# Performance work log

Hardware: AMD Instinct MI355X
Metric: run time of the kernel (lower is better)

## Reference

```python
import jax, jax.numpy as jnp
import numpy as np

R = 16            # grid resolution
WIN = 8           # window size (voxels per side)
NW3 = (R // WIN) ** 3   # number of windows = 8
WS = WIN ** 3           # tokens per window = 512
N = R ** 3              # active voxels = 4096
C = 512; H = 8; DH = C // H; L = 8; LAT = 8
NG = 4; VOX = 0.015625; OUTC = 14 * NG; MLP = 4 * C


def _radical_inverse(base, i):
    f = 1.0; r = 0.0
    while i > 0:
        f /= base; r += f * (i % base); i //= base
    return r


def _offset_perturbation():
    # hammersley_sequence(3, i, NG) = [i/NG, phi_2(i), phi_3(i)]
    p = np.array([[i / NG, _radical_inverse(2, i), _radical_inverse(3, i)] for i in range(NG)], np.float32)
    p = p * 2.0 - 1.0
    p = np.clip(p / VOX, -0.99, 0.99)
    return jnp.asarray(np.arctanh(p).astype(np.float32))  # [NG, 3]


def setup_inputs() -> dict:
    key = jax.random.key(0)
    ks = jax.random.split(key, 12)
    nw = R // WIN
    # window-major voxel ordering: dense 16^3 grid grouped into 8^3 windows
    win = np.stack(np.meshgrid(*[np.arange(nw)] * 3, indexing='ij'), -1).reshape(-1, 3)
    inner = np.stack(np.meshgrid(*[np.arange(WIN)] * 3, indexing='ij'), -1).reshape(-1, 3)
    xyz = (win[:, None, :] * WIN + inner[None, :, :]).reshape(-1, 3).astype(np.int32)
    coords = jnp.asarray(np.concatenate([np.zeros((N, 1), np.int32), xyz], axis=1))  # [N,4] (batch,x,y,z)
    s = 0.02
    return {
        'feats': jax.random.normal(ks[0], (N, LAT), jnp.float32),
        'coords': coords,
        'emb_x': jax.random.normal(ks[1], (1024, C // 3), jnp.float32) * s,
        'emb_y': jax.random.normal(ks[2], (1024, C // 3), jnp.float32) * s,
        'emb_z': jax.random.normal(ks[3], (1024, C - 2 * (C // 3)), jnp.float32) * s,
        'w_in': jax.random.normal(ks[4], (LAT, C), jnp.float32) * s,
        'b_in': jnp.zeros((C,), jnp.float32),
        'ln1_g': jnp.ones((L, C), jnp.float32), 'ln1_b': jnp.zeros((L, C), jnp.float32),
        'w_qkv': jax.random.normal(ks[5], (L, C, 3 * C), jnp.float32) * s,
        'b_qkv': jnp.zeros((L, 3 * C), jnp.float32),
        'w_o': jax.random.normal(ks[6], (L, C, C), jnp.float32) * s,
        'b_o': jnp.zeros((L, C), jnp.float32),
        'ln2_g': jnp.ones((L, C), jnp.float32), 'ln2_b': jnp.zeros((L, C), jnp.float32),
        'w_m1': jax.random.normal(ks[7], (L, C, MLP), jnp.float32) * s,
        'b_m1': jnp.zeros((L, MLP), jnp.float32),
        'w_m2': jax.random.normal(ks[8], (L, MLP, C), jnp.float32) * s,
        'b_m2': jnp.zeros((L, C), jnp.float32),
        'w_out': jax.random.normal(ks[9], (C, OUTC), jnp.float32) * s,
        'b_out': jnp.zeros((OUTC,), jnp.float32),
        'offset_perturb': _offset_perturbation(),
    }


def _ln(x, g, b, eps):
    m = jnp.mean(x, axis=-1, keepdims=True)
    v = jnp.var(x, axis=-1, keepdims=True)
    return (x - m) * jax.lax.rsqrt(v + eps) * g + b


def _forward(feats, coords, emb_x, emb_y, emb_z, w_in, b_in, ln1_g, ln1_b,
             w_qkv, b_qkv, w_o, b_o, ln2_g, ln2_b, w_m1, b_m1, w_m2, b_m2,
             w_out, b_out, offset_perturb):
    # input_layer + absolute position embedding (gather from 3 tables)
    h = feats @ w_in + b_in  # [N, C]
    pe = jnp.concatenate([emb_x[coords[:, 1]], emb_y[coords[:, 2]], emb_z[coords[:, 3]]], axis=-1)
    h = h + pe

    def block(h, p):
        l1g, l1b, wq, bq, wo, bo, l2g, l2b, w1, b1, w2, b2 = p
        a = _ln(h, l1g, l1b, 1e-6)
        qkv = (a @ wq + bq).reshape(NW3, WS, 3, H, DH)  # voxels are window-major
        q, k, v = qkv[:, :, 0], qkv[:, :, 1], qkv[:, :, 2]
        scores = jnp.einsum('wqhd,wkhd->whqk', q, k) / jnp.sqrt(jnp.float32(DH))
        attn = jax.nn.softmax(scores, axis=-1)
        o = jnp.einsum('whqk,wkhd->wqhd', attn, v).reshape(N, C)
        h = h + o @ wo + bo
        m = _ln(h, l2g, l2b, 1e-6)
        h = h + jax.nn.gelu(m @ w1 + b1) @ w2 + b2
        return h, None

    params = (ln1_g, ln1_b, w_qkv, b_qkv, w_o, b_o, ln2_g, ln2_b, w_m1, b_m1, w_m2, b_m2)
    h, _ = jax.lax.scan(block, h, params)

    # final non-affine layer_norm + out projection
    h = _ln(h, jnp.ones((C,), h.dtype), jnp.zeros((C,), h.dtype), 1e-5)
    out = h @ w_out + b_out  # [N, 56]

    # to_representation (single batch)
    xyz_base = (coords[:, 1:].astype(jnp.float32) + 0.5) / R  # [N, 3]
    off = out[:, 0:3 * NG].reshape(N, NG, 3) + offset_perturb
    off = jnp.tanh(off) / R * 0.5 * VOX
    _xyz = (xyz_base[:, None, :] + off).reshape(N * NG, 3)
    _fdc = out[:, 3 * NG:6 * NG].reshape(N * NG, 1, 3)
    _scal = out[:, 6 * NG:9 * NG].reshape(N * NG, 3)
    _rot = out[:, 9 * NG:13 * NG].reshape(N * NG, 4)
    _opa = out[:, 13 * NG:14 * NG].reshape(N * NG, 1)
    return _xyz, _fdc, _scal, _rot, _opa


def reference(feats, coords, emb_x, emb_y, emb_z, w_in, b_in, ln1_g, ln1_b,
              w_qkv, b_qkv, w_o, b_o, ln2_g, ln2_b, w_m1, b_m1, w_m2, b_m2,
              w_out, b_out, offset_perturb):
    return _forward(feats, coords, emb_x, emb_y, emb_z, w_in, b_in, ln1_g, ln1_b,
                    w_qkv, b_qkv, w_o, b_o, ln2_g, ln2_b, w_m1, b_m1, w_m2, b_m2,
                    w_out, b_out, offset_perturb)
```

## Files before the change

### kernel.cpp

```cpp
#include <hip/hip_runtime.h>
#include <stdint.h>

typedef unsigned short u16;
typedef short bf16x8 __attribute__((ext_vector_type(8)));
typedef float f32x4 __attribute__((ext_vector_type(4)));

#define NTOK 4096
#define CDIM 512
#define NHEAD 8
#define LAYERS 8
#define MLPD 2048
#define QKVD 1536

__device__ __forceinline__ u16 f2bf(float f){
  union { float f; unsigned u; } c; c.f = f;
  return (u16)((c.u + 0x7FFFu + ((c.u >> 16) & 1u)) >> 16);
}

__device__ __forceinline__ void llds16(const void* g, void* l){
  __builtin_amdgcn_global_load_lds((const __attribute__((address_space(1))) void*)g,
                                   (__attribute__((address_space(3))) void*)l, 16, 0, 0);
}

__global__ void kt_transpose(const float* __restrict__ W, u16* __restrict__ Wt, int K, int N){
  __shared__ float tile[32][33];
  int l = blockIdx.z;
  W  += (size_t)l * K * N;
  Wt += (size_t)l * K * N;
  int k0 = blockIdx.y * 32, n0 = blockIdx.x * 32;
  int t = threadIdx.x;
  int r = t >> 3, c4 = (t & 7) << 2;
  float4 v = *(const float4*)&W[(size_t)(k0 + r) * N + n0 + c4];
  tile[r][c4 + 0] = v.x; tile[r][c4 + 1] = v.y; tile[r][c4 + 2] = v.z; tile[r][c4 + 3] = v.w;
  __syncthreads();
  ushort4 o;
  o.x = f2bf(tile[c4 + 0][r]);
  o.y = f2bf(tile[c4 + 1][r]);
  o.z = f2bf(tile[c4 + 2][r]);
  o.w = f2bf(tile[c4 + 3][r]);
  *(ushort4*)&Wt[(size_t)(n0 + r) * K + k0 + c4] = o;
}

__global__ void kt_embed(const float* __restrict__ feats, const int* __restrict__ coords,
                         const float* __restrict__ ex, const float* __restrict__ ey,
                         const float* __restrict__ ez, const float* __restrict__ w_in,
                         const float* __restrict__ b_in, float* __restrict__ h){
  __shared__ float fs[8];
  __shared__ int cc[3];
  int n = blockIdx.x, t = threadIdx.x;
  if (t < 8) fs[t] = feats[n * 8 + t];
  if (t == 8) { cc[0] = coords[n*4+1]; cc[1] = coords[n*4+2]; cc[2] = coords[n*4+3]; }
  __syncthreads();
  for (int c = t; c < CDIM; c += 256){
    float acc = b_in[c];
    #pragma unroll
    for (int i = 0; i < 8; i++) acc += fs[i] * w_in[i * CDIM + c];
    float pe;
    if (c < 170)      pe = ex[cc[0] * 170 + c];
    else if (c < 340) pe = ey[cc[1] * 170 + (c - 170)];
    else              pe = ez[cc[2] * 172 + (c - 340)];
    h[(size_t)n * CDIM + c] = acc + pe;
  }
}

__global__ void kt_ln(const float* __restrict__ h, const float* __restrict__ g,
                      const float* __restrict__ b, u16* __restrict__ out, float eps){
  int wave = threadIdx.x >> 6, lane = threadIdx.x & 63;
  int row = blockIdx.x * 4 + wave;
  const float* hr = h + (size_t)row * CDIM + lane * 8;
  float4 v0 = *(const float4*)hr, v1 = *(const float4*)(hr + 4);
  float x[8] = {v0.x, v0.y, v0.z, v0.w, v1.x, v1.y, v1.z, v1.w};
  float s = 0.f, q = 0.f;
  #pragma unroll
  for (int i = 0; i < 8; i++){ s += x[i]; q += x[i] * x[i]; }
  #pragma unroll
  for (int off = 32; off; off >>= 1){ s += __shfl_xor(s, off); q += __shfl_xor(q, off); }
  float mean = s * (1.0f / CDIM);
  float var  = q * (1.0f / CDIM) - mean * mean;
  float rr = rsqrtf(var + eps);
  int cb = lane * 8;
  u16 u[8];
  #pragma unroll
  for (int i = 0; i < 8; i++)
    u[i] = f2bf((x[i] - mean) * rr * g[cb + i] + b[cb + i]);
  uint4 pk;
  pk.x = (unsigned)u[0] | ((unsigned)u[1] << 16);
  pk.y = (unsigned)u[2] | ((unsigned)u[3] << 16);
  pk.z = (unsigned)u[4] | ((unsigned)u[5] << 16);
  pk.w = (unsigned)u[6] | ((unsigned)u[7] << 16);
  *(uint4*)&out[(size_t)row * CDIM + cb] = pk;
}

template<int BM, int BN, int MODE>
__global__ __launch_bounds__(256) void kt_gemm(
    const u16* __restrict__ A, const u16* __restrict__ Wt, const float* __restrict__ bias,
    u16* __restrict__ outb, float* __restrict__ hres, u16* __restrict__ vT, int N, int K)
{
  constexpr int MF = BM / 32;
  constexpr int NF = BN / 32;
  __shared__ __align__(16) u16 As[2][BM * 64];
  __shared__ __align__(16) u16 Bs[2][BN * 64];
  int tid = threadIdx.x, wave = tid >> 6, lane = tid & 63;
  int m0 = blockIdx.y * BM, n0 = blockIdx.x * BN;
  int wm = wave >> 1, wn = wave & 1;
  f32x4 acc[MF][NF];
  const f32x4 fzero = {0.f, 0.f, 0.f, 0.f};
  #pragma unroll
  for (int m = 0; m < MF; m++)
    #pragma unroll
    for (int n = 0; n < NF; n++) acc[m][n] = fzero;

  int srow = lane >> 3;
  int sblk = (lane & 7) ^ srow;
  const u16* gA = A  + (size_t)(m0 + wave * 8 + srow) * K + sblk * 8;
  const u16* gB = Wt + (size_t)(n0 + wave * 8 + srow) * K + sblk * 8;

  auto stage = [&](int buf, int kt){
    #pragma unroll
    for (int j = 0; j < BM / 32; j++)
      llds16(gA + (size_t)(j * 32) * K + kt, &As[buf][(j * 32 + wave * 8) * 64]);
    #pragma unroll
    for (int j = 0; j < BN / 32; j++)
      llds16(gB + (size_t)(j * 32) * K + kt, &Bs[buf][(j * 32 + wave * 8) * 64]);
  };

  int nk = K >> 6;
  stage(0, 0);
  __syncthreads();
  int rl = lane & 15, hg = lane >> 4;
  for (int t = 0; t < nk; ++t){
    int cur = t & 1;
    if (t + 1 < nk) stage(cur ^ 1, (t + 1) << 6);
    #pragma unroll
    for (int kk = 0; kk < 2; kk++){
      bf16x8 af[MF], bfr[NF];
      int bl = (kk << 2) + hg;
      #pragma unroll
      for (int m = 0; m < MF; m++){
        int row = wm * (BM / 2) + m * 16 + rl;
        af[m] = *(const bf16x8*)&As[cur][row * 64 + ((bl ^ (row & 7)) << 3)];
      }
      #pragma unroll
      for (int n = 0; n < NF; n++){
        int row = wn * (BN / 2) + n * 16 + rl;
        bfr[n] = *(const bf16x8*)&Bs[cur][row * 64 + ((bl ^ (row & 7)) << 3)];
      }
      #pragma unroll
      for (int m = 0; m < MF; m++)
        #pragma unroll
        for (int n = 0; n < NF; n++)
          acc[m][n] = __builtin_amdgcn_mfma_f32_16x16x32_bf16(af[m], bfr[n], acc[m][n], 0, 0, 0);
    }
    __syncthreads();
  }

  int cl = lane & 15, rg = lane >> 4;
  #pragma unroll
  for (int m = 0; m < MF; m++){
    int row0 = m0 + wm * (BM / 2) + m * 16 + rg * 4;
    #pragma unroll
    for (int n = 0; n < NF; n++){
      int col = n0 + wn * (BN / 2) + n * 16 + cl;
      float bb = bias[col];
      if (MODE == 1){
        #pragma unroll
        for (int r = 0; r < 4; r++){
          size_t idx = (size_t)(row0 + r) * N + col;
          hres[idx] += acc[m][n][r] + bb;
        }
      } else if (MODE == 2){
        #pragma unroll
        for (int r = 0; r < 4; r++){
          float x = acc[m][n][r] + bb;
          float t = 0.7978845608028654f * (x + 0.044715f * x * x * x);
          outb[(size_t)(row0 + r) * N + col] = f2bf(0.5f * x * (1.0f + tanhf(t)));
        }
      } else {
        if (col < 1024){
          #pragma unroll
          for (int r = 0; r < 4; r++)
            outb[(size_t)(row0 + r) * N + col] = f2bf(acc[m][n][r] + bb);
        } else {
          int dh = col - 1024;
          int win = row0 >> 9, tin = row0 & 511;
          ushort4 p;
          p.x = f2bf(acc[m][n][0] + bb);
          p.y = f2bf(acc[m][n][1] + bb);
          p.z = f2bf(acc[m][n][2] + bb);
          p.w = f2bf(acc[m][n][3] + bb);
          *(ushort4*)&vT[(size_t)(win * 512 + dh) * 512 + tin] = p;
        }
      }
    }
  }
}

__global__ __launch_bounds__(256) void kt_attn(const u16* __restrict__ qkv,
                                               const u16* __restrict__ vT,
                                               u16* __restrict__ o){
  __shared__ __align__(16) u16 P[4][32 * 32];
  int tid = threadIdx.x, wave = tid >> 6, lane = tid & 63;
  int qc = blockIdx.x, head = blockIdx.y, win = blockIdx.z;
  int rl = lane & 15, hg = lane >> 4;
  int qbase = win * 512 + qc * 128 + wave * 32;
  const u16* qptr = qkv + (size_t)qbase * QKVD + head * 64;
  const u16* kptr = qkv + (size_t)(win * 512) * QKVD + 512 + head * 64;
  const u16* vptr = vT + (size_t)(win * 512 + head * 64) * 512;
  u16* Pl = &P[wave][0];

  bf16x8 qf[2][2];
  #pragma unroll
  for (int m = 0; m < 2; m++)
    #pragma unroll
    for (int kk = 0; kk < 2; kk++)
      qf[m][kk] = *(const bf16x8*)(qptr + (size_t)(m * 16 + rl) * QKVD + kk * 32 + hg * 8);

  const f32x4 fzero = {0.f, 0.f, 0.f, 0.f};
  f32x4 Oa[2][4];
  float mrun[2][4], lrun[2][4];
  #pragma unroll
  for (int m = 0; m < 2; m++){
    #pragma unroll
    for (int d = 0; d < 4; d++) Oa[m][d] = fzero;
    #pragma unroll
    for (int r = 0; r < 4; r++){ mrun[m][r] = -1e30f; lrun[m][r] = 0.f; }
  }

  for (int kt = 0; kt < 512; kt += 32){
    f32x4 s[2][2];
    #pragma unroll
    for (int m = 0; m < 2; m++){ s[m][0] = fzero; s[m][1] = fzero; }
    #pragma unroll
    for (int c = 0; c < 2; c++){
      bf16x8 kf0 = *(const bf16x8*)(kptr + (size_t)(kt + c * 16 + rl) * QKVD + hg * 8);
      bf16x8 kf1 = *(const bf16x8*)(kptr + (size_t)(kt + c * 16 + rl) * QKVD + 32 + hg * 8);
      #pragma unroll
      for (int m = 0; m < 2; m++){
        s[m][c] = __builtin_amdgcn_mfma_f32_16x16x32_bf16(qf[m][0], kf0, s[m][c], 0, 0, 0);
        s[m][c] = __builtin_amdgcn_mfma_f32_16x16x32_bf16(qf[m][1], kf1, s[m][c], 0, 0, 0);
      }
    }
    bf16x8 vf[4];
    #pragma unroll
    for (int d = 0; d < 4; d++)
      vf[d] = *(const bf16x8*)(vptr + (size_t)(d * 16 + rl) * 512 + kt + hg * 8);

    #pragma unroll
    for (int m = 0; m < 2; m++){
      #pragma unroll
      for (int r = 0; r < 4; r++){
        float s0 = s[m][0][r] * 0.125f, s1 = s[m][1][r] * 0.125f;
        float mx = fmaxf(s0, s1);
        #pragma unroll
        for (int off = 1; off < 16; off <<= 1) mx = fmaxf(mx, __shfl_xor(mx, off));
        float mnew = fmaxf(mrun[m][r], mx);
        float corr = __expf(mrun[m][r] - mnew);
        mrun[m][r] = mnew;
        float p0 = __expf(s0 - mnew), p1 = __expf(s1 - mnew);
        float ps = p0 + p1;
        #pragma unroll
        for (int off = 1; off < 16; off <<= 1) ps += __shfl_xor(ps, off);
        lrun[m][r] = lrun[m][r] * corr + ps;
        #pragma unroll
        for (int d = 0; d < 4; d++) Oa[m][d][r] *= corr;
        s[m][0][r] = p0; s[m][1][r] = p1;
      }
    }
    #pragma unroll
    for (int m = 0; m < 2; m++)
      #pragma unroll
      for (int c = 0; c < 2; c++)
        #pragma unroll
        for (int r = 0; r < 4; r++){
          int row = m * 16 + hg * 4 + r;
          int colb = c * 2 + (rl >> 3);
          Pl[row * 32 + ((colb ^ (row & 3)) << 3) + (rl & 7)] = f2bf(s[m][c][r]);
        }
    __syncthreads();
    #pragma unroll
    for (int m = 0; m < 2; m++){
      int prow = m * 16 + rl;
      bf16x8 pf = *(const bf16x8*)&Pl[prow * 32 + ((hg ^ (prow & 3)) << 3)];
      #pragma unroll
      for (int d = 0; d < 4; d++)
        Oa[m][d] = __builtin_amdgcn_mfma_f32_16x16x32_bf16(pf, vf[d], Oa[m][d], 0, 0, 0);
    }
    __syncthreads();
  }
  #pragma unroll
  for (int m = 0; m < 2; m++)
    #pragma unroll
    for (int d = 0; d < 4; d++)
      #pragma unroll
      for (int r = 0; r < 4; r++){
        int row = qbase + m * 16 + hg * 4 + r;
        o[(size_t)row * CDIM + head * 64 + d * 16 + rl] = f2bf(Oa[m][d][r] / lrun[m][r]);
      }
}

__global__ void kt_final(const float* __restrict__ h, const float* __restrict__ w_out,
                         const float* __restrict__ b_out, const int* __restrict__ coords,
                         const float* __restrict__ offp, float* __restrict__ out){
  __shared__ float lnv[CDIM];
  __shared__ float ov[56];
  int n = blockIdx.x, lane = threadIdx.x;
  const float* hr = h + (size_t)n * CDIM + lane * 8;
  float4 v0 = *(const float4*)hr, v1 = *(const float4*)(hr + 4);
  float x[8] = {v0.x, v0.y, v0.z, v0.w, v1.x, v1.y, v1.z, v1.w};
  float s = 0.f, q = 0.f;
  #pragma unroll
  for (int i = 0; i < 8; i++){ s += x[i]; q += x[i] * x[i]; }
  #pragma unroll
  for (int off = 32; off; off >>= 1){ s += __shfl_xor(s, off); q += __shfl_xor(q, off); }
  float mean = s * (1.0f / CDIM);
  float var  = q * (1.0f / CDIM) - mean * mean;
  float rr = rsqrtf(var + 1e-5f);
  #pragma unroll
  for (int i = 0; i < 8; i++) lnv[lane * 8 + i] = (x[i] - mean) * rr;
  __syncthreads();
  if (lane < 56){
    float a = b_out[lane];
    for (int k = 0; k < CDIM; k++) a += lnv[k] * w_out[k * 56 + lane];
    ov[lane] = a;
  }
  __syncthreads();
  if (lane < 12){
    int g = lane / 3, d = lane - g * 3;
    float base = ((float)coords[n * 4 + 1 + d] + 0.5f) * (1.0f / 16.0f);
    float t = tanhf(ov[lane] + offp[lane]);
    out[(size_t)n * 12 + lane] = base + t * 4.8828125e-4f;
    out[49152  + (size_t)n * 12 + lane] = ov[12 + lane];
    out[98304  + (size_t)n * 12 + lane] = ov[24 + lane];
  }
  if (lane < 16) out[147456 + (size_t)n * 16 + lane] = ov[36 + lane];
  if (lane < 4)  out[212992 + (size_t)n * 4  + lane] = ov[52 + lane];
}

extern "C" void kernel_launch(void* const* d_in, const int* in_sizes, int n_in,
                              void* d_out, int out_size, void* d_ws, size_t ws_size,
                              hipStream_t stream) {
  const float* feats = (const float*)d_in[0];
  const int*   coords = (const int*)d_in[1];
  const float* emb_x = (const float*)d_in[2];
  const float* emb_y = (const float*)d_in[3];
  const float* emb_z = (const float*)d_in[4];
  const float* w_in  = (const float*)d_in[5];
  const float* b_in  = (const float*)d_in[6];
  const float* ln1_g = (const float*)d_in[7];
  const float* ln1_b = (const float*)d_in[8];
  const float* w_qkv = (const float*)d_in[9];
  const float* b_qkv = (const float*)d_in[10];
  const float* w_o   = (const float*)d_in[11];
  const float* b_o   = (const float*)d_in[12];
  const float* ln2_g = (const float*)d_in[13];
  const float* ln2_b = (const float*)d_in[14];
  const float* w_m1  = (const float*)d_in[15];
  const float* b_m1  = (const float*)d_in[16];
  const float* w_m2  = (const float*)d_in[17];
  const float* b_m2  = (const float*)d_in[18];
  const float* w_out = (const float*)d_in[19];
  const float* b_out = (const float*)d_in[20];
  const float* offp  = (const float*)d_in[21];

  char* ws = (char*)d_ws;
  auto carve = [&](size_t bytes){ char* p = ws; ws += (bytes + 255) & ~(size_t)255; return p; };
  float* h   = (float*)carve((size_t)NTOK * CDIM * 4);
  u16* a     = (u16*)carve((size_t)NTOK * CDIM * 2);
  u16* qkvb  = (u16*)carve((size_t)NTOK * QKVD * 2);
  u16* vT    = (u16*)carve((size_t)NTOK * CDIM * 2);
  u16* ob    = (u16*)carve((size_t)NTOK * CDIM * 2);
  u16* ub    = (u16*)carve((size_t)NTOK * MLPD * 2);
  u16* wqkvT = (u16*)carve((size_t)LAYERS * QKVD * CDIM * 2);
  u16* woT   = (u16*)carve((size_t)LAYERS * CDIM * CDIM * 2);
  u16* wm1T  = (u16*)carve((size_t)LAYERS * MLPD * CDIM * 2);
  u16* wm2T  = (u16*)carve((size_t)LAYERS * CDIM * MLPD * 2);

  kt_transpose<<<dim3(QKVD/32, CDIM/32, LAYERS), 256, 0, stream>>>(w_qkv, wqkvT, CDIM, QKVD);
  kt_transpose<<<dim3(CDIM/32, CDIM/32, LAYERS), 256, 0, stream>>>(w_o,   woT,   CDIM, CDIM);
  kt_transpose<<<dim3(MLPD/32, CDIM/32, LAYERS), 256, 0, stream>>>(w_m1,  wm1T,  CDIM, MLPD);
  kt_transpose<<<dim3(CDIM/32, MLPD/32, LAYERS), 256, 0, stream>>>(w_m2,  wm2T,  MLPD, CDIM);
  kt_embed<<<NTOK, 256, 0, stream>>>(feats, coords, emb_x, emb_y, emb_z, w_in, b_in, h);

  for (int l = 0; l < LAYERS; ++l){
    kt_ln<<<NTOK/4, 256, 0, stream>>>(h, ln1_g + l*CDIM, ln1_b + l*CDIM, a, 1e-6f);
    kt_gemm<64,128,0><<<dim3(QKVD/128, NTOK/64), 256, 0, stream>>>(
        a, wqkvT + (size_t)l*QKVD*CDIM, b_qkv + l*QKVD, qkvb, nullptr, vT, QKVD, CDIM);
    kt_attn<<<dim3(4, NHEAD, 8), 256, 0, stream>>>(qkvb, vT, ob);
    kt_gemm<64,64,1><<<dim3(CDIM/64, NTOK/64), 256, 0, stream>>>(
        ob, woT + (size_t)l*CDIM*CDIM, b_o + l*CDIM, nullptr, h, nullptr, CDIM, CDIM);
    kt_ln<<<NTOK/4, 256, 0, stream>>>(h, ln2_g + l*CDIM, ln2_b + l*CDIM, a, 1e-6f);
    kt_gemm<64,128,2><<<dim3(MLPD/128, NTOK/64), 256, 0, stream>>>(
        a, wm1T + (size_t)l*MLPD*CDIM, b_m1 + l*MLPD, ub, nullptr, nullptr, MLPD, CDIM);
    kt_gemm<64,64,1><<<dim3(CDIM/64, NTOK/64), 256, 0, stream>>>(
        ub, wm2T + (size_t)l*CDIM*MLPD, b_m2 + l*CDIM, nullptr, h, nullptr, CDIM, MLPD);
  }
  kt_final<<<NTOK, 64, 0, stream>>>(h, w_out, b_out, coords, offp, (float*)d_out);
}
```

Baseline: 1.019 ms.

## Restructure attention: 16-row waves, transposed S, register P shuffle, double-buffered K/V

The attention kernel now gives each wave a 16-query tile instead of 32, which raises the grid from 256 to 512 blocks (2048 wave tasks) for better occupancy. S is computed transposed (K as the A operand) so the per-row max and sum reductions need only two cross-lane shuffles. The P matrix is rearranged into the MFMA operand layout through register shuffles, removing the LDS staging buffer and both __syncthreads per tile. K and V fragments are double-buffered in registers to overlap global loads with compute. In exchange, each K/V fragment is reloaded by twice as many waves, and the shuffle-based layout is easy to get wrong.

```diff
diff --git a/kernel.cpp b/kernel.cpp
--- a/kernel.cpp
+++ b/kernel.cpp
@@ -15,6 +15,10 @@
 __device__ __forceinline__ u16 f2bf(float f){
   union { float f; unsigned u; } c; c.f = f;
   return (u16)((c.u + 0x7FFFu + ((c.u >> 16) & 1u)) >> 16);
+}
+
+__device__ __forceinline__ unsigned pack2(float a, float b){
+  return (unsigned)f2bf(a) | ((unsigned)f2bf(b) << 16);
 }
 
 __device__ __forceinline__ void llds16(const void* g, void* l){
@@ -198,104 +202,111 @@
 __global__ __launch_bounds__(256) void kt_attn(const u16* __restrict__ qkv,
                                                const u16* __restrict__ vT,
                                                u16* __restrict__ o){
-  __shared__ __align__(16) u16 P[4][32 * 32];
   int tid = threadIdx.x, wave = tid >> 6, lane = tid & 63;
-  int qc = blockIdx.x, head = blockIdx.y, win = blockIdx.z;
+  int task = blockIdx.x * 4 + wave;
+  int qc = task & 31, head = (task >> 5) & 7, win = task >> 8;
   int rl = lane & 15, hg = lane >> 4;
-  int qbase = win * 512 + qc * 128 + wave * 32;
-  const u16* qptr = qkv + (size_t)qbase * QKVD + head * 64;
+  int qbase = win * 512 + qc * 16;
+  const u16* qptr = qkv + (size_t)(qbase + rl) * QKVD + head * 64;
   const u16* kptr = qkv + (size_t)(win * 512) * QKVD + 512 + head * 64;
   const u16* vptr = vT + (size_t)(win * 512 + head * 64) * 512;
-  u16* Pl = &P[wave][0];
-
-  bf16x8 qf[2][2];
-  #pragma unroll
-  for (int m = 0; m < 2; m++)
-    #pragma unroll
-    for (int kk = 0; kk < 2; kk++)
-      qf[m][kk] = *(const bf16x8*)(qptr + (size_t)(m * 16 + rl) * QKVD + kk * 32 + hg * 8);
+
+  bf16x8 qf0 = *(const bf16x8*)(qptr + hg * 8);
+  bf16x8 qf1 = *(const bf16x8*)(qptr + 32 + hg * 8);
 
   const f32x4 fzero = {0.f, 0.f, 0.f, 0.f};
-  f32x4 Oa[2][4];
-  float mrun[2][4], lrun[2][4];
-  #pragma unroll
-  for (int m = 0; m < 2; m++){
-    #pragma unroll
-    for (int d = 0; d < 4; d++) Oa[m][d] = fzero;
-    #pragma unroll
-    for (int r = 0; r < 4; r++){ mrun[m][r] = -1e30f; lrun[m][r] = 0.f; }
-  }
-
-  for (int kt = 0; kt < 512; kt += 32){
-    f32x4 s[2][2];
-    #pragma unroll
-    for (int m = 0; m < 2; m++){ s[m][0] = fzero; s[m][1] = fzero; }
-    #pragma unroll
-    for (int c = 0; c < 2; c++){
-      bf16x8 kf0 = *(const bf16x8*)(kptr + (size_t)(kt + c * 16 + rl) * QKVD + hg * 8);
-      bf16x8 kf1 = *(const bf16x8*)(kptr + (size_t)(kt + c * 16 + rl) * QKVD + 32 + hg * 8);
+  f32x4 Oa[4] = {fzero, fzero, fzero, fzero};
+  float mrun = -1e30f, lrun = 0.f;
+
+  bf16x8 kA[2][2], vA[4], kB[2][2], vB[4];
+
+  auto loadK = [&](int kt, bf16x8 kf[2][2]){
+    #pragma unroll
+    for (int c = 0; c < 2; c++)
       #pragma unroll
-      for (int m = 0; m < 2; m++){
-        s[m][c] = __builtin_amdgcn_mfma_f32_16x16x32_bf16(qf[m][0], kf0, s[m][c], 0, 0, 0);
-        s[m][c] = __builtin_amdgcn_mfma_f32_16x16x32_bf16(qf[m][1], kf1, s[m][c], 0, 0, 0);
-      }
-    }
-    bf16x8 vf[4];
+      for (int dk = 0; dk < 2; dk++)
+        kf[c][dk] = *(const bf16x8*)(kptr + (size_t)(kt + c * 16 + rl) * QKVD + dk * 32 + hg * 8);
+  };
+  auto loadV = [&](int kt, bf16x8 vf[4]){
     #pragma unroll
     for (int d = 0; d < 4; d++)
       vf[d] = *(const bf16x8*)(vptr + (size_t)(d * 16 + rl) * 512 + kt + hg * 8);
-
-    #pragma unroll
-    for (int m = 0; m < 2; m++){
-      #pragma unroll
-      for (int r = 0; r < 4; r++){
-        float s0 = s[m][0][r] * 0.125f, s1 = s[m][1][r] * 0.125f;
-        float mx = fmaxf(s0, s1);
-        #pragma unroll
-        for (int off = 1; off < 16; off <<= 1) mx = fmaxf(mx, __shfl_xor(mx, off));
-        float mnew = fmaxf(mrun[m][r], mx);
-        float corr = __expf(mrun[m][r] - mnew);
-        mrun[m][r] = mnew;
-        float p0 = __expf(s0 - mnew), p1 = __expf(s1 - mnew);
-        float ps = p0 + p1;
-        #pragma unroll
-        for (int off = 1; off < 16; off <<= 1) ps += __shfl_xor(ps, off);
-        lrun[m][r] = lrun[m][r] * corr + ps;
-        #pragma unroll
-        for (int d = 0; d < 4; d++) Oa[m][d][r] *= corr;
-        s[m][0][r] = p0; s[m][1][r] = p1;
-      }
+  };
+
+  auto process = [&](bf16x8 kf[2][2], bf16x8 vf[4]){
+    f32x4 s0 = fzero, s1 = fzero;
+    s0 = __builtin_amdgcn_mfma_f32_16x16x32_bf16(kf[0][0], qf0, s0, 0, 0, 0);
+    s0 = __builtin_amdgcn_mfma_f32_16x16x32_bf16(kf[0][1], qf1, s0, 0, 0, 0);
+    s1 = __builtin_amdgcn_mfma_f32_16x16x32_bf16(kf[1][0], qf0, s1, 0, 0, 0);
+    s1 = __builtin_amdgcn_mfma_f32_16x16x32_bf16(kf[1][1], qf1, s1, 0, 0, 0);
+    float v[8];
+    #pragma unroll
+    for (int r = 0; r < 4; r++){ v[r] = s0[r] * 0.125f; v[4 + r] = s1[r] * 0.125f; }
+    float tmax = v[0];
+    #pragma unroll
+    for (int i = 1; i < 8; i++) tmax = fmaxf(tmax, v[i]);
+    tmax = fmaxf(tmax, __shfl_xor(tmax, 16));
+    tmax = fmaxf(tmax, __shfl_xor(tmax, 32));
+    float mnew = fmaxf(mrun, tmax);
+    float corr = __expf(mrun - mnew);
+    mrun = mnew;
+    float p[8], ps = 0.f;
+    #pragma unroll
+    for (int i = 0; i < 8; i++){ p[i] = __expf(v[i] - mnew); ps += p[i]; }
+    ps += __shfl_xor(ps, 16);
+    ps += __shfl_xor(ps, 32);
+    lrun = lrun * corr + ps;
+    float c0 = __shfl(corr, (hg << 2) + 0);
+    float c1 = __shfl(corr, (hg << 2) + 1);
+    float c2 = __shfl(corr, (hg << 2) + 2);
+    float c3 = __shfl(corr, (hg << 2) + 3);
+    #pragma unroll
+    for (int d = 0; d < 4; d++){
+      Oa[d][0] *= c0; Oa[d][1] *= c1; Oa[d][2] *= c2; Oa[d][3] *= c3;
     }
-    #pragma unroll
-    for (int m = 0; m < 2; m++)
-      #pragma unroll
-      for (int c = 0; c < 2; c++)
-        #pragma unroll
-        for (int r = 0; r < 4; r++){
-          int row = m * 16 + hg * 4 + r;
-          int colb = c * 2 + (rl >> 3);
-          Pl[row * 32 + ((colb ^ (row & 3)) << 3) + (rl & 7)] = f2bf(s[m][c][r]);
-        }
-    __syncthreads();
-    #pragma unroll
-    for (int m = 0; m < 2; m++){
-      int prow = m * 16 + rl;
-      bf16x8 pf = *(const bf16x8*)&Pl[prow * 32 + ((hg ^ (prow & 3)) << 3)];
-      #pragma unroll
-      for (int d = 0; d < 4; d++)
-        Oa[m][d] = __builtin_amdgcn_mfma_f32_16x16x32_bf16(pf, vf[d], Oa[m][d], 0, 0, 0);
+    unsigned pk00 = pack2(p[0], p[1]);
+    unsigned pk01 = pack2(p[2], p[3]);
+    unsigned pk10 = pack2(p[4], p[5]);
+    unsigned pk11 = pack2(p[6], p[7]);
+    int idx0 = rl | ((( hg << 1)      & 3) << 4);
+    int idx1 = rl | ((((hg << 1) + 1) & 3) << 4);
+    bool hiC = hg >= 2;
+    unsigned W0a = __shfl(pk00, idx0), W0b = __shfl(pk10, idx0);
+    unsigned W1a = __shfl(pk01, idx0), W1b = __shfl(pk11, idx0);
+    unsigned W2a = __shfl(pk00, idx1), W2b = __shfl(pk10, idx1);
+    unsigned W3a = __shfl(pk01, idx1), W3b = __shfl(pk11, idx1);
+    uint4 W;
+    W.x = hiC ? W0b : W0a;
+    W.y = hiC ? W1b : W1a;
+    W.z = hiC ? W2b : W2a;
+    W.w = hiC ? W3b : W3a;
+    bf16x8 pf;
+    __builtin_memcpy(&pf, &W, 16);
+    #pragma unroll
+    for (int d = 0; d < 4; d++)
+      Oa[d] = __builtin_amdgcn_mfma_f32_16x16x32_bf16(pf, vf[d], Oa[d], 0, 0, 0);
+  };
+
+  loadK(0, kA); loadV(0, vA);
+  for (int kt = 0; kt < 512; kt += 64){
+    loadK(kt + 32, kB); loadV(kt + 32, vB);
+    process(kA, vA);
+    if (kt + 64 < 512){ loadK(kt + 64, kA); loadV(kt + 64, vA); }
+    process(kB, vB);
+  }
+
+  float l0 = __shfl(lrun, (hg << 2) + 0);
+  float l1 = __shfl(lrun, (hg << 2) + 1);
+  float l2 = __shfl(lrun, (hg << 2) + 2);
+  float l3 = __shfl(lrun, (hg << 2) + 3);
+  float li[4] = {1.f / l0, 1.f / l1, 1.f / l2, 1.f / l3};
+  #pragma unroll
+  for (int d = 0; d < 4; d++)
+    #pragma unroll
+    for (int r = 0; r < 4; r++){
+      int row = qbase + (hg << 2) + r;
+      o[(size_t)row * CDIM + head * 64 + d * 16 + rl] = f2bf(Oa[d][r] * li[r]);
     }
-    __syncthreads();
-  }
-  #pragma unroll
-  for (int m = 0; m < 2; m++)
-    #pragma unroll
-    for (int d = 0; d < 4; d++)
-      #pragma unroll
-      for (int r = 0; r < 4; r++){
-        int row = qbase + m * 16 + hg * 4 + r;
-        o[(size_t)row * CDIM + head * 64 + d * 16 + rl] = f2bf(Oa[m][d][r] / lrun[m][r]);
-      }
 }
 
 __global__ void kt_final(const float* __restrict__ h, const float* __restrict__ w_out,
@@ -385,7 +396,7 @@
     kt_ln<<<NTOK/4, 256, 0, stream>>>(h, ln1_g + l*CDIM, ln1_b + l*CDIM, a, 1e-6f);
     kt_gemm<64,128,0><<<dim3(QKVD/128, NTOK/64), 256, 0, stream>>>(
         a, wqkvT + (size_t)l*QKVD*CDIM, b_qkv + l*QKVD, qkvb, nullptr, vT, QKVD, CDIM);
-    kt_attn<<<dim3(4, NHEAD, 8), 256, 0, stream>>>(qkvb, vT, ob);
+    kt_attn<<<512, 256, 0, stream>>>(qkvb, vT, ob);
     kt_gemm<64,64,1><<<dim3(CDIM/64, NTOK/64), 256, 0, stream>>>(
         ob, woT + (size_t)l*CDIM*CDIM, b_o + l*CDIM, nullptr, h, nullptr, CDIM, CDIM);
     kt_ln<<<NTOK/4, 256, 0, stream>>>(h, ln2_g + l*CDIM, ln2_b + l*CDIM, a, 1e-6f);
```

Result: faster. 978.3 us (-4.0%).
